# Performance work log

Hardware: AMD Instinct MI355X
Metric: run time of the kernel (lower is better)

## Reference

```python
import jax, jax.numpy as jnp
import numpy as np

GRID = 64
BIG = 1.0e6  # threshold pushing masked-out pixels to huge distance


def _grid_dist(grid_h, grid_w):
    # pairwise euclidean distance between all grid points, (H, W, H, W)
    xs, ys = jnp.meshgrid(jnp.arange(grid_h), jnp.arange(grid_w), indexing='ij')
    coords = jnp.stack([xs.ravel(), ys.ravel()], axis=-1).astype(jnp.float32)  # (H*W, 2)
    d = jnp.sqrt(jnp.sum((coords[:, None, :] - coords[None, :, :]) ** 2, axis=-1))
    return d.reshape(grid_h, grid_w, grid_h, grid_w)


def setup_inputs() -> dict:
    key = jax.random.key(0)
    k1, k2 = jax.random.split(key)
    gt = jax.random.uniform(k1, (8, 64, 64), dtype=jnp.float32)
    pred = jax.random.uniform(k2, (8, 64, 64), dtype=jnp.float32)
    return {"gt": gt, "pred": pred}


def reference(gt, pred):
    # mode='l2_sq': sum over last axis (W for a (B,H,W) mask), then mean
    loss = jnp.mean(jnp.sum((gt - pred) ** 2, axis=-1))

    # affinity loss (dist_mat += 1.0 as in the original)
    dist = _grid_dist(GRID, GRID) + 1.0  # (64,64,64,64)

    gt_th = gt + (1.0 - gt) * BIG      # (B,H,W)
    pred_th = pred + (1.0 - pred) * BIG

    # dist_masked[b,h,w,i,j] = gt_th[b,h,w] * dist[h,w,i,j] * pred[b,i,j]
    dist_masked = gt_th[:, :, :, None, None] * dist[None] * pred[:, None, None, :, :]
    min_dist = jnp.mean(jnp.min(dist_masked, axis=(3, 4)))

    dist_masked_inv = pred_th[:, :, :, None, None] * dist[None] * gt[:, None, None, :, :]
    min_dist_inv = jnp.mean(jnp.min(dist_masked_inv, axis=(3, 4)))

    return (loss, min_dist, min_dist_inv)
```

## Files before the change

kernel.cpp:

```cpp
#include <hip/hip_runtime.h>

#define BIGV 1.0e6f

__device__ __forceinline__ float wave_max64(float v) {
    #pragma unroll
    for (int s = 32; s > 0; s >>= 1)
        v = fmaxf(v, __shfl_xor(v, s, 64));
    return v;
}

__global__ __launch_bounds__(64) void imageloss_bnb2(
    const float* __restrict__ gt, const float* __restrict__ pred,
    float* __restrict__ ws, float* __restrict__ out)
{
    __shared__ float img[4096];

    const int blk   = blockIdx.x;
    const int patch = blk & 63;
    const int dir   = (blk >> 6) & 1;
    const int b     = blk >> 7;
    const int lane  = threadIdx.x;

    const float* __restrict__ src = (dir ? gt : pred) + b * 4096;

    #pragma unroll
    for (int k = 0; k < 16; ++k)
        ((float4*)img)[k * 64 + lane] = ((const float4*)src)[k * 64 + lane];
    __syncthreads();

    const int ti = lane >> 3, tj = lane & 7;
    float tmin_l;
    {
        const float* tp = img + ti * 512 + tj * 8;
        float t0 = 1e30f, t1 = 1e30f;
        #pragma unroll
        for (int r = 0; r < 8; ++r) {
            float4 a = *(const float4*)(tp + r * 64);
            float4 c = *(const float4*)(tp + r * 64 + 4);
            t0 = fminf(t0, fminf(fminf(a.x, a.y), fminf(a.z, a.w)));
            t1 = fminf(t1, fminf(fminf(c.x, c.y), fminf(c.z, c.w)));
        }
        tmin_l = fminf(t0, t1);
    }

    const int Pi = patch >> 3, Pj = patch & 7;
    const int qi = Pi * 8 + (lane >> 3);
    const int qj = Pj * 8 + (lane & 7);
    const float qif = (float)qi, qjf = (float)qj;

    float ma = 3.4e38f, mb = 3.4e38f;

    auto eval_tile = [&](int tti, int ttj) {
        const float* tpx = img + tti * 512 + ttj * 8;
        float4 va[8], vb[8];
        #pragma unroll
        for (int r = 0; r < 8; ++r) {
            va[r] = *(const float4*)(tpx + r * 64);
            vb[r] = *(const float4*)(tpx + r * 64 + 4);
        }
        #pragma unroll
        for (int r = 0; r < 8; ++r) {
            const float ddx = qif - (float)(tti * 8 + r);
            const float dx2 = ddx * ddx;
            #pragma unroll
            for (int cc = 0; cc < 4; ++cc) {
                const float dyA = qjf - (float)(ttj * 8 + cc);
                const float dyB = qjf - (float)(ttj * 8 + 4 + cc);
                const float dA = __builtin_amdgcn_sqrtf(fmaf(dyA, dyA, dx2));
                const float dB = __builtin_amdgcn_sqrtf(fmaf(dyB, dyB, dx2));
                const float vA = (&va[r].x)[cc], vB = (&vb[r].x)[cc];
                ma = fminf(ma, fmaf(vA, dA, vA));
                mb = fminf(mb, fmaf(vB, dB, vB));
            }
        }
    };

    unsigned long long nearmask = 0;
    #pragma unroll
    for (int di = -1; di <= 1; ++di) {
        #pragma unroll
        for (int dj = -1; dj <= 1; ++dj) {
            const int t2i = Pi + di, t2j = Pj + dj;
            if ((unsigned)t2i < 8u && (unsigned)t2j < 8u) {
                nearmask |= 1ull << (t2i * 8 + t2j);
                eval_tile(t2i, t2j);
            }
        }
    }

    int adti = ti - Pi; adti = adti < 0 ? -adti : adti;
    int adtj = tj - Pj; adtj = adtj < 0 ? -adtj : adtj;
    const int rho_l = adti > adtj ? adti : adtj;
    const float gx = fmaxf((float)(adti * 8 - 7), 0.0f);
    const float gy = fmaxf((float)(adtj * 8 - 7), 0.0f);
    const float dbox = __builtin_amdgcn_sqrtf(fmaf(gx, gx, gy * gy));
    const float bnd = fmaf(tmin_l, dbox, tmin_l);

    float M = wave_max64(fminf(ma, mb));
    unsigned long long remaining = __ballot(bnd < M) & ~nearmask;

    for (int rho = 2; rho <= 7 && remaining; ++rho) {
        unsigned long long cur = remaining & __ballot(rho_l == rho);
        while (cur) {
            const int t = (int)__builtin_ctzll(cur);
            const unsigned long long bit = 1ull << t;
            cur &= ~bit; remaining &= ~bit;
            eval_tile(t >> 3, t & 7);
            M = wave_max64(fminf(ma, mb));
            const unsigned long long alive = __ballot(bnd < M);
            cur &= alive; remaining &= alive;
        }
    }
    const float m = fminf(ma, mb);

    const int cell = b * 4096 + qi * 64 + qj;
    const float own = img[qi * 64 + qj];

    float c12, sq = 0.0f;
    if (dir == 0) {
        const float g = gt[cell];
        const float gth = g + (1.0f - g) * BIGV;
        c12 = gth * m;
        const float df = g - own;
        sq = df * df;
    } else {
        const float p = pred[cell];
        const float pth = p + (1.0f - p) * BIGV;
        c12 = pth * m;
    }

    #pragma unroll
    for (int off = 32; off > 0; off >>= 1) {
        c12 += __shfl_down(c12, off, 64);
        sq  += __shfl_down(sq,  off, 64);
    }
    if (lane == 0) {
        if (dir == 0) {
            atomicAdd(&ws[0], sq);
            atomicAdd(&ws[1], c12);
        } else {
            atomicAdd(&ws[2], c12);
        }
        __threadfence();
        const int old = atomicAdd((int*)&ws[3], 1);
        if (old == 1023) {
            const float s0 = atomicAdd(&ws[0], 0.0f);
            const float s1 = atomicAdd(&ws[1], 0.0f);
            const float s2 = atomicAdd(&ws[2], 0.0f);
            out[0] = s0 * (1.0f / 512.0f);
            out[1] = s1 * (1.0f / 32768.0f);
            out[2] = s2 * (1.0f / 32768.0f);
        }
    }
}

extern "C" void kernel_launch(void* const* d_in, const int* in_sizes, int n_in,
                              void* d_out, int out_size, void* d_ws, size_t ws_size,
                              hipStream_t stream)
{
    const float* gt   = (const float*)d_in[0];
    const float* pred = (const float*)d_in[1];
    float* out = (float*)d_out;
    float* ws  = (float*)d_ws;

    hipMemsetAsync(ws, 0, 4 * sizeof(float), stream);
    imageloss_bnb2<<<1024, 64, 0, stream>>>(gt, pred, ws, out);
}
```

Measured before the change: 48.74 us.

## Split per-patch tile search across four waves per block

Each block now runs four wavefronts instead of one. The near-neighbour tiles and the remaining far tiles of the branch-and-bound search are split across the waves, and partial minima are combined through shared memory. The aim is to shorten each block's serial tile evaluation and raise per-CU parallelism. In exchange it adds two block barriers, wave-local pruning that uses a less tight bound after the split, and lower block-level occupancy per CU.

```diff
diff --git a/kernel.cpp b/kernel.cpp
--- a/kernel.cpp
+++ b/kernel.cpp
@@ -9,23 +9,26 @@
     return v;
 }
 
-__global__ __launch_bounds__(64) void imageloss_bnb2(
+__global__ __launch_bounds__(256) void imageloss_bnb3(
     const float* __restrict__ gt, const float* __restrict__ pred,
     float* __restrict__ ws, float* __restrict__ out)
 {
     __shared__ float img[4096];
+    __shared__ float red[4][64];
 
     const int blk   = blockIdx.x;
     const int patch = blk & 63;
     const int dir   = (blk >> 6) & 1;
     const int b     = blk >> 7;
-    const int lane  = threadIdx.x;
+    const int tid   = threadIdx.x;
+    const int wv    = tid >> 6;
+    const int lane  = tid & 63;
 
     const float* __restrict__ src = (dir ? gt : pred) + b * 4096;
 
     #pragma unroll
-    for (int k = 0; k < 16; ++k)
-        ((float4*)img)[k * 64 + lane] = ((const float4*)src)[k * 64 + lane];
+    for (int k = 0; k < 4; ++k)
+        ((float4*)img)[k * 256 + tid] = ((const float4*)src)[k * 256 + tid];
     __syncthreads();
 
     const int ti = lane >> 3, tj = lane & 7;
@@ -44,8 +47,8 @@
     }
 
     const int Pi = patch >> 3, Pj = patch & 7;
-    const int qi = Pi * 8 + (lane >> 3);
-    const int qj = Pj * 8 + (lane & 7);
+    const int qi = Pi * 8 + ti;
+    const int qj = Pj * 8 + tj;
     const float qif = (float)qi, qjf = (float)qj;
 
     float ma = 3.4e38f, mb = 3.4e38f;
@@ -76,6 +79,7 @@
     };
 
     unsigned long long nearmask = 0;
+    int nidx = 0;
     #pragma unroll
     for (int di = -1; di <= 1; ++di) {
         #pragma unroll
@@ -83,10 +87,17 @@
             const int t2i = Pi + di, t2j = Pj + dj;
             if ((unsigned)t2i < 8u && (unsigned)t2j < 8u) {
                 nearmask |= 1ull << (t2i * 8 + t2j);
-                eval_tile(t2i, t2j);
+                if ((nidx & 3) == wv) eval_tile(t2i, t2j);
+                ++nidx;
             }
         }
     }
+
+    red[wv][lane] = fminf(ma, mb);
+    __syncthreads();
+    const float mcomb = fminf(fminf(red[0][lane], red[1][lane]),
+                              fminf(red[2][lane], red[3][lane]));
+    ma = mcomb; mb = 3.4e38f;
 
     int adti = ti - Pi; adti = adti < 0 ? -adti : adti;
     int adtj = tj - Pj; adtj = adtj < 0 ? -adtj : adtj;
@@ -96,8 +107,9 @@
     const float dbox = __builtin_amdgcn_sqrtf(fmaf(gx, gx, gy * gy));
     const float bnd = fmaf(tmin_l, dbox, tmin_l);
 
-    float M = wave_max64(fminf(ma, mb));
-    unsigned long long remaining = __ballot(bnd < M) & ~nearmask;
+    const unsigned long long wavesel = 0x1111111111111111ull << wv;
+    float M = wave_max64(ma);
+    unsigned long long remaining = __ballot(bnd < M) & ~nearmask & wavesel;
 
     for (int rho = 2; rho <= 7 && remaining; ++rho) {
         unsigned long long cur = remaining & __ballot(rho_l == rho);
@@ -111,45 +123,52 @@
             cur &= alive; remaining &= alive;
         }
     }
-    const float m = fminf(ma, mb);
 
-    const int cell = b * 4096 + qi * 64 + qj;
-    const float own = img[qi * 64 + qj];
+    red[wv][lane] = fminf(ma, mb);
+    __syncthreads();
 
-    float c12, sq = 0.0f;
-    if (dir == 0) {
-        const float g = gt[cell];
-        const float gth = g + (1.0f - g) * BIGV;
-        c12 = gth * m;
-        const float df = g - own;
-        sq = df * df;
-    } else {
-        const float p = pred[cell];
-        const float pth = p + (1.0f - p) * BIGV;
-        c12 = pth * m;
-    }
+    if (wv == 0) {
+        const float m = fminf(fminf(red[0][lane], red[1][lane]),
+                              fminf(red[2][lane], red[3][lane]));
 
-    #pragma unroll
-    for (int off = 32; off > 0; off >>= 1) {
-        c12 += __shfl_down(c12, off, 64);
-        sq  += __shfl_down(sq,  off, 64);
-    }
-    if (lane == 0) {
+        const int cell = b * 4096 + qi * 64 + qj;
+        const float own = img[qi * 64 + qj];
+
+        float c12, sq = 0.0f;
         if (dir == 0) {
-            atomicAdd(&ws[0], sq);
-            atomicAdd(&ws[1], c12);
+            const float g = gt[cell];
+            const float gth = g + (1.0f - g) * BIGV;
+            c12 = gth * m;
+            const float df = g - own;
+            sq = df * df;
         } else {
-            atomicAdd(&ws[2], c12);
+            const float p = pred[cell];
+            const float pth = p + (1.0f - p) * BIGV;
+            c12 = pth * m;
         }
-        __threadfence();
-        const int old = atomicAdd((int*)&ws[3], 1);
-        if (old == 1023) {
-            const float s0 = atomicAdd(&ws[0], 0.0f);
-            const float s1 = atomicAdd(&ws[1], 0.0f);
-            const float s2 = atomicAdd(&ws[2], 0.0f);
-            out[0] = s0 * (1.0f / 512.0f);
-            out[1] = s1 * (1.0f / 32768.0f);
-            out[2] = s2 * (1.0f / 32768.0f);
+
+        #pragma unroll
+        for (int off = 32; off > 0; off >>= 1) {
+            c12 += __shfl_down(c12, off, 64);
+            sq  += __shfl_down(sq,  off, 64);
+        }
+        if (lane == 0) {
+            if (dir == 0) {
+                atomicAdd(&ws[0], sq);
+                atomicAdd(&ws[1], c12);
+            } else {
+                atomicAdd(&ws[2], c12);
+            }
+            __threadfence();
+            const int old = atomicAdd((int*)&ws[3], 1);
+            if (old == 1023) {
+                const float s0 = atomicAdd(&ws[0], 0.0f);
+                const float s1 = atomicAdd(&ws[1], 0.0f);
+                const float s2 = atomicAdd(&ws[2], 0.0f);
+                out[0] = s0 * (1.0f / 512.0f);
+                out[1] = s1 * (1.0f / 32768.0f);
+                out[2] = s2 * (1.0f / 32768.0f);
+            }
         }
     }
 }
@@ -164,5 +183,5 @@
     float* ws  = (float*)d_ws;
 
     hipMemsetAsync(ws, 0, 4 * sizeof(float), stream);
-    imageloss_bnb2<<<1024, 64, 0, stream>>>(gt, pred, ws, out);
+    imageloss_bnb3<<<1024, 256, 0, stream>>>(gt, pred, ws, out);
 }
```

Measured after the change: 47.38 us. 1.03x faster.
